# Performance work log

Hardware: AMD Instinct MI355X
Metric: run time of the kernel (lower is better)

## Reference

```python
import jax, jax.numpy as jnp
import numpy as np

N_NODES = 50000
BN_EPS = 1e-5


def setup_inputs() -> dict:
    key = jax.random.key(0)
    ks = jax.random.split(key, 10)
    n, e, d, L = N_NODES, 500000, 128, 2
    x = jax.random.normal(ks[0], (n, d), dtype=jnp.float32)
    edge_index = jax.random.randint(ks[1], (2, e), 0, n, dtype=jnp.int64)
    edge_attr = jax.random.normal(ks[2], (e, d), dtype=jnp.float32)
    W1 = jax.random.normal(ks[3], (L, d, d), dtype=jnp.float32) * 0.05
    b1 = jax.random.normal(ks[4], (L, d), dtype=jnp.float32) * 0.02
    gamma = 1.0 + 0.1 * jax.random.normal(ks[5], (L, d), dtype=jnp.float32)
    beta = 0.1 * jax.random.normal(ks[6], (L, d), dtype=jnp.float32)
    W2 = jax.random.normal(ks[7], (L, d, d), dtype=jnp.float32) * 0.05
    b2 = jax.random.normal(ks[8], (L, d), dtype=jnp.float32) * 0.02
    return {"x": x, "edge_index": edge_index, "edge_attr": edge_attr,
            "W1": W1, "b1": b1, "gamma": gamma, "beta": beta, "W2": W2, "b2": b2}


def _gine_layer(x, src, dst, edge_attr, W1l, b1l, gl, bl, W2l, b2l):
    # GINEConv message: relu(x_j + edge_attr), sum-aggregated to target nodes
    msg = jax.nn.relu(x[src] + edge_attr)              # [E, d]
    agg = jax.ops.segment_sum(msg, dst, num_segments=N_NODES)  # [N, d]
    h = (x + agg) @ W1l + b1l                           # eps=0 -> (1+eps)*x = x
    # BatchNorm1d over nodes (train-mode batch stats, biased var)
    mu = jnp.mean(h, axis=0)
    var = jnp.mean(jnp.square(h - mu), axis=0)
    h = (h - mu) * jax.lax.rsqrt(var + BN_EPS) * gl + bl
    h = jax.nn.relu(h)
    h = jax.nn.relu(h @ W2l + b2l)
    return jax.nn.relu(h)  # encoder's outer activation


def reference(x, edge_index, edge_attr, W1, b1, gamma, beta, W2, b2):
    src, dst = edge_index[0], edge_index[1]
    L = W1.shape[0]
    for l in range(L):
        x = _gine_layer(x, src, dst, edge_attr, W1[l], b1[l], gamma[l], beta[l], W2[l], b2[l])
    return x
```

## Files before the change

### kernel.cpp

```cpp
#include <hip/hip_runtime.h>

#define BN_EPS 1e-5f

using f4 = __attribute__((ext_vector_type(4))) float;
using h4 = __attribute__((ext_vector_type(4))) _Float16;

__device__ inline f4 relu4(f4 v) {
    v.x = fmaxf(v.x, 0.f); v.y = fmaxf(v.y, 0.f);
    v.z = fmaxf(v.z, 0.f); v.w = fmaxf(v.w, 0.f);
    return v;
}

__global__ __launch_bounds__(256) void detect_i64_kernel(const int* __restrict__ ei,
                                                         int* __restrict__ flag, int npairs,
                                                         int* __restrict__ deg, int N) {
    __shared__ int ok;
    if (threadIdx.x == 0) ok = 1;
    __syncthreads();
    bool bad = false;
    for (int i = threadIdx.x; i < npairs; i += 256)
        bad |= (ei[2 * i + 1] != 0);
    if (bad) ok = 0;
    int nq = N >> 2;
    int4* d4 = (int4*)deg;
    for (int i = threadIdx.x; i < nq; i += 256) d4[i] = make_int4(0, 0, 0, 0);
    for (int i = (nq << 2) + threadIdx.x; i < N; i += 256) deg[i] = 0;
    __syncthreads();
    if (threadIdx.x == 0) *flag = ok;
}

__global__ __launch_bounds__(256) void canon_kernel(const int* __restrict__ ei,
                                                    const int* __restrict__ flag,
                                                    int* __restrict__ canon,
                                                    int* __restrict__ deg, int n2, int E) {
    int i = blockIdx.x * 256 + threadIdx.x;
    if (i >= n2) return;
    int wide = *flag;
    int v = wide ? ei[2 * i] : ei[i];
    canon[i] = v;
    if (i >= E) atomicAdd(&deg[v], 1);
}

__global__ __launch_bounds__(256) void scan_blk_kernel(const int* __restrict__ deg,
                                                       int* __restrict__ rowptr,
                                                       int* __restrict__ partials, int N) {
    __shared__ int s[256];
    int b = blockIdx.x, t = threadIdx.x;
    int base = b * 1024 + t * 4;
    int4 v = make_int4(0, 0, 0, 0);
    if (base + 3 < N) v = *(const int4*)(deg + base);
    else {
        if (base < N) v.x = deg[base];
        if (base + 1 < N) v.y = deg[base + 1];
        if (base + 2 < N) v.z = deg[base + 2];
        if (base + 3 < N) v.w = deg[base + 3];
    }
    s[t] = v.x + v.y + v.z + v.w;
    __syncthreads();
    for (int off = 1; off < 256; off <<= 1) {
        int u = (t >= off) ? s[t - off] : 0;
        __syncthreads();
        s[t] += u;
        __syncthreads();
    }
    int excl = (t == 0) ? 0 : s[t - 1];
    int4 w;
    w.x = excl;
    w.y = excl + v.x;
    w.z = w.y + v.y;
    w.w = w.z + v.z;
    if (base + 3 < N) *(int4*)(rowptr + base) = w;
    else {
        if (base < N) rowptr[base] = w.x;
        if (base + 1 < N) rowptr[base + 1] = w.y;
        if (base + 2 < N) rowptr[base + 2] = w.z;
        if (base + 3 < N) rowptr[base + 3] = w.w;
    }
    if (t == 255) partials[b] = s[255];
}

__global__ __launch_bounds__(256) void scan_part_kernel(int* __restrict__ partials, int nb) {
    __shared__ int s[256];
    int t = threadIdx.x;
    if (nb <= 256) {
        s[t] = (t < nb) ? partials[t] : 0;
        __syncthreads();
        for (int off = 1; off < 256; off <<= 1) {
            int u = (t >= off) ? s[t - off] : 0;
            __syncthreads();
            s[t] += u;
            __syncthreads();
        }
        if (t < nb) partials[t] = (t == 0) ? 0 : s[t - 1];
    } else if (t == 0) {
        int run = 0;
        for (int i = 0; i < nb; ++i) { int d = partials[i]; partials[i] = run; run += d; }
    }
}

__global__ __launch_bounds__(256) void scan_add_kernel(int* __restrict__ rowptr,
                                                       int* __restrict__ cursor,
                                                       const int* __restrict__ partials,
                                                       float* __restrict__ sums, int nsum,
                                                       int N, int E) {
    int i = blockIdx.x * 256 + threadIdx.x;
    if (i < nsum) sums[i] = 0.f;
    if (i < N) {
        int v = rowptr[i] + partials[i >> 10];
        rowptr[i] = v;
        cursor[i] = v;
    }
    if (i == N) rowptr[N] = E;
}

__global__ __launch_bounds__(256) void fill_kernel(const int* __restrict__ src,
                                                   const int* __restrict__ dst,
                                                   int* __restrict__ cursor,
                                                   int2* __restrict__ pbuf, int E) {
    int e = blockIdx.x * 256 + threadIdx.x;
    if (e >= E) return;
    int d = dst[e];
    int pos = atomicAdd(&cursor[d], 1);
    pbuf[pos] = make_int2(e, src[e]);
}

template <int EAH>
__global__ __launch_bounds__(256) void gg1_kernel(const float* __restrict__ x,
                                                  const float* __restrict__ ea,
                                                  _Float16* __restrict__ eah,
                                                  const int* __restrict__ rowptr,
                                                  const int2* __restrict__ pbuf,
                                                  const float* __restrict__ W,
                                                  const float* __restrict__ bias,
                                                  float* __restrict__ sums,
                                                  float* __restrict__ out, int N) {
    __shared__ float sA[64][132];
    __shared__ float sW[32][128];
    int t = threadIdx.x;
    int rbase = blockIdx.x * 64;
    int f = t & 31, g = t >> 5;

    for (int it = 0; it < 8; ++it) {
        int r = g * 8 + it;
        int n = rbase + r;
        f4 acc0 = {0.f, 0.f, 0.f, 0.f};
        f4 acc1 = {0.f, 0.f, 0.f, 0.f};
        f4 acc2 = {0.f, 0.f, 0.f, 0.f};
        f4 acc3 = {0.f, 0.f, 0.f, 0.f};
        if (n < N) {
            acc0 = ((const f4*)(x + (size_t)n * 128))[f];
            int lo = rowptr[n], hi = rowptr[n + 1];
            int i = lo;
            if (EAH == 1) {
                const h4* ep = (const h4*)eah;
                for (; i + 4 <= hi; i += 4) {
                    int2 q0 = pbuf[i];
                    int2 q1 = pbuf[i + 1];
                    int2 q2 = pbuf[i + 2];
                    int2 q3 = pbuf[i + 3];
                    f4 xa = ((const f4*)(x + (size_t)q0.y * 128))[f];
                    h4 ha = __builtin_nontemporal_load(ep + (size_t)i * 32 + f);
                    f4 xb = ((const f4*)(x + (size_t)q1.y * 128))[f];
                    h4 hb = __builtin_nontemporal_load(ep + (size_t)(i + 1) * 32 + f);
                    f4 xc = ((const f4*)(x + (size_t)q2.y * 128))[f];
                    h4 hc = __builtin_nontemporal_load(ep + (size_t)(i + 2) * 32 + f);
                    f4 xd = ((const f4*)(x + (size_t)q3.y * 128))[f];
                    h4 hd = __builtin_nontemporal_load(ep + (size_t)(i + 3) * 32 + f);
                    acc0 += relu4(xa + __builtin_convertvector(ha, f4));
                    acc1 += relu4(xb + __builtin_convertvector(hb, f4));
                    acc2 += relu4(xc + __builtin_convertvector(hc, f4));
                    acc3 += relu4(xd + __builtin_convertvector(hd, f4));
                }
                for (; i < hi; ++i) {
                    int2 q0 = pbuf[i];
                    f4 xa = ((const f4*)(x + (size_t)q0.y * 128))[f];
                    h4 ha = __builtin_nontemporal_load(ep + (size_t)i * 32 + f);
                    acc0 += relu4(xa + __builtin_convertvector(ha, f4));
                }
            } else {
                for (; i + 4 <= hi; i += 4) {
                    int2 q0 = pbuf[i];
                    int2 q1 = pbuf[i + 1];
                    int2 q2 = pbuf[i + 2];
                    int2 q3 = pbuf[i + 3];
                    f4 xa = ((const f4*)(x + (size_t)q0.y * 128))[f];
                    f4 aa = __builtin_nontemporal_load(((const f4*)(ea + (size_t)q0.x * 128)) + f);
                    f4 xb = ((const f4*)(x + (size_t)q1.y * 128))[f];
                    f4 ab = __builtin_nontemporal_load(((const f4*)(ea + (size_t)q1.x * 128)) + f);
                    f4 xc = ((const f4*)(x + (size_t)q2.y * 128))[f];
                    f4 ac = __builtin_nontemporal_load(((const f4*)(ea + (size_t)q2.x * 128)) + f);
                    f4 xd = ((const f4*)(x + (size_t)q3.y * 128))[f];
                    f4 ad = __builtin_nontemporal_load(((const f4*)(ea + (size_t)q3.x * 128)) + f);
                    if (EAH == 0) {
                        h4* ep = (h4*)eah;
                        __builtin_nontemporal_store(__builtin_convertvector(aa, h4), ep + (size_t)i * 32 + f);
                        __builtin_nontemporal_store(__builtin_convertvector(ab, h4), ep + (size_t)(i + 1) * 32 + f);
                        __builtin_nontemporal_store(__builtin_convertvector(ac, h4), ep + (size_t)(i + 2) * 32 + f);
                        __builtin_nontemporal_store(__builtin_convertvector(ad, h4), ep + (size_t)(i + 3) * 32 + f);
                    }
                    acc0 += relu4(xa + aa);
                    acc1 += relu4(xb + ab);
                    acc2 += relu4(xc + ac);
                    acc3 += relu4(xd + ad);
                }
                for (; i < hi; ++i) {
                    int2 q0 = pbuf[i];
                    f4 xa = ((const f4*)(x + (size_t)q0.y * 128))[f];
                    f4 aa = __builtin_nontemporal_load(((const f4*)(ea + (size_t)q0.x * 128)) + f);
                    if (EAH == 0) {
                        h4* ep = (h4*)eah;
                        __builtin_nontemporal_store(__builtin_convertvector(aa, h4), ep + (size_t)i * 32 + f);
                    }
                    acc0 += relu4(xa + aa);
                }
            }
        }
        f4 rv = (acc0 + acc1) + (acc2 + acc3);
        *(f4*)&sA[r][f * 4] = rv;
    }

    float acc[4][8];
#pragma unroll
    for (int r = 0; r < 4; ++r)
#pragma unroll
        for (int c = 0; c < 8; ++c) acc[r][c] = 0.f;

    int cg = t & 15, rg = t >> 4;
    int c0a = cg * 4;
    int c0b = 64 + cg * 4;

    for (int kc = 0; kc < 4; ++kc) {
        __syncthreads();
#pragma unroll
        for (int pass = 0; pass < 4; ++pass) {
            int kk = (t >> 5) + pass * 8;
            int k = kc * 32 + kk;
            float4 w = reinterpret_cast<const float4*>(W + (size_t)k * 128)[t & 31];
            *reinterpret_cast<float4*>(&sW[kk][(t & 31) * 4]) = w;
        }
        __syncthreads();
#pragma unroll
        for (int kk0 = 0; kk0 < 32; kk0 += 4) {
            float4 a[4];
#pragma unroll
            for (int r = 0; r < 4; ++r)
                a[r] = *reinterpret_cast<const float4*>(&sA[rg * 4 + r][kc * 32 + kk0]);
#pragma unroll
            for (int j = 0; j < 4; ++j) {
                float4 w0 = *reinterpret_cast<const float4*>(&sW[kk0 + j][c0a]);
                float4 w1 = *reinterpret_cast<const float4*>(&sW[kk0 + j][c0b]);
#pragma unroll
                for (int r = 0; r < 4; ++r) {
                    float av = (j == 0) ? a[r].x : (j == 1) ? a[r].y : (j == 2) ? a[r].z : a[r].w;
                    acc[r][0] += av * w0.x;
                    acc[r][1] += av * w0.y;
                    acc[r][2] += av * w0.z;
                    acc[r][3] += av * w0.w;
                    acc[r][4] += av * w1.x;
                    acc[r][5] += av * w1.y;
                    acc[r][6] += av * w1.z;
                    acc[r][7] += av * w1.w;
                }
            }
        }
    }

    float4 b0 = *reinterpret_cast<const float4*>(bias + c0a);
    float4 b1v = *reinterpret_cast<const float4*>(bias + c0b);
    float cs[8], cs2[8];
#pragma unroll
    for (int j = 0; j < 8; ++j) { cs[j] = 0.f; cs2[j] = 0.f; }

#pragma unroll
    for (int r = 0; r < 4; ++r) {
        int row = rbase + rg * 4 + r;
        if (row >= N) continue;
        float4 o0, o1;
        o0.x = acc[r][0] + b0.x;  o0.y = acc[r][1] + b0.y;
        o0.z = acc[r][2] + b0.z;  o0.w = acc[r][3] + b0.w;
        o1.x = acc[r][4] + b1v.x; o1.y = acc[r][5] + b1v.y;
        o1.z = acc[r][6] + b1v.z; o1.w = acc[r][7] + b1v.w;
        cs[0] += o0.x; cs2[0] += o0.x * o0.x;
        cs[1] += o0.y; cs2[1] += o0.y * o0.y;
        cs[2] += o0.z; cs2[2] += o0.z * o0.z;
        cs[3] += o0.w; cs2[3] += o0.w * o0.w;
        cs[4] += o1.x; cs2[4] += o1.x * o1.x;
        cs[5] += o1.y; cs2[5] += o1.y * o1.y;
        cs[6] += o1.z; cs2[6] += o1.z * o1.z;
        cs[7] += o1.w; cs2[7] += o1.w * o1.w;
        *reinterpret_cast<float4*>(out + (size_t)row * 128 + c0a) = o0;
        *reinterpret_cast<float4*>(out + (size_t)row * 128 + c0b) = o1;
    }

    __syncthreads();
    float* red = &sA[0][0];
    float* red2 = red + 2048;
    int base = (rg * 16 + cg) * 8;
#pragma unroll
    for (int j = 0; j < 8; ++j) { red[base + j] = cs[j]; red2[base + j] = cs2[j]; }
    __syncthreads();
    if (t < 128) {
        int cgj = (t & 63) >> 2;
        int j = (t & 3) + ((t >> 6) << 2);
        float s = 0.f, s2 = 0.f;
#pragma unroll
        for (int rr = 0; rr < 16; ++rr) {
            s += red[(rr * 16 + cgj) * 8 + j];
            s2 += red2[(rr * 16 + cgj) * 8 + j];
        }
        unsafeAtomicAdd(&sums[t], s);
        unsafeAtomicAdd(&sums[128 + t], s2);
    }
}

__global__ __launch_bounds__(256) void gemm2_kernel(const float* __restrict__ A,
                                                    const float* __restrict__ W,
                                                    const float* __restrict__ bias,
                                                    const float* __restrict__ sums,
                                                    const float* __restrict__ gamma,
                                                    const float* __restrict__ beta,
                                                    float* __restrict__ out, int N,
                                                    float invN) {
    __shared__ float sA[64][132];
    __shared__ float sW[32][128];
    __shared__ float sScale[128];
    __shared__ float sShift[128];
    int t = threadIdx.x;
    int rbase = blockIdx.x * 64;

    if (t < 128) {
        float mean = sums[t] * invN;
        float var = sums[128 + t] * invN - mean * mean;
        float inv = rsqrtf(var + BN_EPS);
        float sc = gamma[t] * inv;
        sScale[t] = sc;
        sShift[t] = beta[t] - mean * sc;
    }
    __syncthreads();

    {
        int colq = t & 31;
        int r0 = t >> 5;
        float4 s4 = reinterpret_cast<const float4*>(sScale)[colq];
        float4 sh4 = reinterpret_cast<const float4*>(sShift)[colq];
#pragma unroll
        for (int it = 0; it < 8; ++it) {
            int r = r0 + it * 8;
            int row = rbase + r;
            float4 v = make_float4(0.f, 0.f, 0.f, 0.f);
            if (row < N) {
                float4 a = reinterpret_cast<const float4*>(A + (size_t)row * 128)[colq];
                v.x = fmaxf(a.x * s4.x + sh4.x, 0.f);
                v.y = fmaxf(a.y * s4.y + sh4.y, 0.f);
                v.z = fmaxf(a.z * s4.z + sh4.z, 0.f);
                v.w = fmaxf(a.w * s4.w + sh4.w, 0.f);
            }
            *reinterpret_cast<float4*>(&sA[r][colq * 4]) = v;
        }
    }

    float acc[4][8];
#pragma unroll
    for (int r = 0; r < 4; ++r)
#pragma unroll
        for (int c = 0; c < 8; ++c) acc[r][c] = 0.f;

    int cg = t & 15, rg = t >> 4;
    int c0a = cg * 4;
    int c0b = 64 + cg * 4;

    for (int kc = 0; kc < 4; ++kc) {
        __syncthreads();
#pragma unroll
        for (int pass = 0; pass < 4; ++pass) {
            int kk = (t >> 5) + pass * 8;
            int k = kc * 32 + kk;
            float4 w = reinterpret_cast<const float4*>(W + (size_t)k * 128)[t & 31];
            *reinterpret_cast<float4*>(&sW[kk][(t & 31) * 4]) = w;
        }
        __syncthreads();
#pragma unroll
        for (int kk0 = 0; kk0 < 32; kk0 += 4) {
            float4 a[4];
#pragma unroll
            for (int r = 0; r < 4; ++r)
                a[r] = *reinterpret_cast<const float4*>(&sA[rg * 4 + r][kc * 32 + kk0]);
#pragma unroll
            for (int j = 0; j < 4; ++j) {
                float4 w0 = *reinterpret_cast<const float4*>(&sW[kk0 + j][c0a]);
                float4 w1 = *reinterpret_cast<const float4*>(&sW[kk0 + j][c0b]);
#pragma unroll
                for (int r = 0; r < 4; ++r) {
                    float av = (j == 0) ? a[r].x : (j == 1) ? a[r].y : (j == 2) ? a[r].z : a[r].w;
                    acc[r][0] += av * w0.x;
                    acc[r][1] += av * w0.y;
                    acc[r][2] += av * w0.z;
                    acc[r][3] += av * w0.w;
                    acc[r][4] += av * w1.x;
                    acc[r][5] += av * w1.y;
                    acc[r][6] += av * w1.z;
                    acc[r][7] += av * w1.w;
                }
            }
        }
    }

    float4 b0 = *reinterpret_cast<const float4*>(bias + c0a);
    float4 b1v = *reinterpret_cast<const float4*>(bias + c0b);
#pragma unroll
    for (int r = 0; r < 4; ++r) {
        int row = rbase + rg * 4 + r;
        if (row >= N) continue;
        float4 o0, o1;
        o0.x = fmaxf(acc[r][0] + b0.x, 0.f);  o0.y = fmaxf(acc[r][1] + b0.y, 0.f);
        o0.z = fmaxf(acc[r][2] + b0.z, 0.f);  o0.w = fmaxf(acc[r][3] + b0.w, 0.f);
        o1.x = fmaxf(acc[r][4] + b1v.x, 0.f); o1.y = fmaxf(acc[r][5] + b1v.y, 0.f);
        o1.z = fmaxf(acc[r][6] + b1v.z, 0.f); o1.w = fmaxf(acc[r][7] + b1v.w, 0.f);
        *reinterpret_cast<float4*>(out + (size_t)row * 128 + c0a) = o0;
        *reinterpret_cast<float4*>(out + (size_t)row * 128 + c0b) = o1;
    }
}

extern "C" void kernel_launch(void* const* d_in, const int* in_sizes, int n_in,
                              void* d_out, int out_size, void* d_ws, size_t ws_size,
                              hipStream_t stream) {
    const float* x     = (const float*)d_in[0];
    const int*   ei    = (const int*)d_in[1];
    const float* ea    = (const float*)d_in[2];
    const float* W1    = (const float*)d_in[3];
    const float* b1    = (const float*)d_in[4];
    const float* gamma = (const float*)d_in[5];
    const float* beta  = (const float*)d_in[6];
    const float* W2    = (const float*)d_in[7];
    const float* b2    = (const float*)d_in[8];

    int N = in_sizes[0] / 128;
    int E = in_sizes[2] / 128;
    int L = in_sizes[3] / (128 * 128);

    size_t NF = (size_t)N * 128;
    float*     h      = (float*)d_ws;
    float*     sums   = h + NF;
    _Float16*  eah    = (_Float16*)(sums + 256 * L);
    int*       canon  = (int*)(eah + (size_t)E * 128);
    int*       deg    = canon + (size_t)2 * E;
    int*       rowptr = deg + N;
    int*       cursor = rowptr + N + 2;
    int2*      pbuf   = (int2*)(cursor + N);
    int*       partials = (int*)(pbuf + E);
    int*       flag   = partials + ((N + 1023) / 1024) + 1;

    int npairs = (E < 4096) ? E : 4096;
    detect_i64_kernel<<<1, 256, 0, stream>>>(ei, flag, npairs, deg, N);
    int E2 = 2 * E;
    canon_kernel<<<(E2 + 255) / 256, 256, 0, stream>>>(ei, flag, canon, deg, E2, E);
    const int* src = canon;
    const int* dst = canon + E;

    int nb = (N + 1023) / 1024;
    scan_blk_kernel<<<nb, 256, 0, stream>>>(deg, rowptr, partials, N);
    scan_part_kernel<<<1, 256, 0, stream>>>(partials, nb);
    scan_add_kernel<<<(N + 256) / 256, 256, 0, stream>>>(rowptr, cursor, partials,
                                                         sums, 256 * L, N, E);
    int eBlocks = (E + 255) / 256;
    fill_kernel<<<eBlocks, 256, 0, stream>>>(src, dst, cursor, pbuf, E);

    int gemmBlocks = (N + 63) / 64;
    float invN = 1.0f / (float)N;
    const float* xin = x;
    for (int l = 0; l < L; ++l) {
        float* xout = (float*)d_out;
        const float* W1l = W1 + (size_t)l * 16384;
        const float* b1l = b1 + (size_t)l * 128;
        float* sums_l = sums + (size_t)l * 256;
        if (l == 0) {
            if (L > 1)
                gg1_kernel<0><<<gemmBlocks, 256, 0, stream>>>(xin, ea, eah, rowptr, pbuf,
                                                              W1l, b1l, sums_l, h, N);
            else
                gg1_kernel<2><<<gemmBlocks, 256, 0, stream>>>(xin, ea, eah, rowptr, pbuf,
                                                              W1l, b1l, sums_l, h, N);
        } else {
            gg1_kernel<1><<<gemmBlocks, 256, 0, stream>>>(xin, ea, eah, rowptr, pbuf,
                                                          W1l, b1l, sums_l, h, N);
        }
        gemm2_kernel<<<gemmBlocks, 256, 0, stream>>>(h, W2 + (size_t)l * 16384,
                                                     b2 + (size_t)l * 128, sums_l,
                                                     gamma + (size_t)l * 128,
                                                     beta + (size_t)l * 128, xout, N, invN);
        xin = xout;
    }
}
```

Measured before the change: 708.1 us.

## Split fused gather-GEMM into gather, permute, and standalone GEMM kernels

```diff
diff --git a/kernel.cpp b/kernel.cpp
--- a/kernel.cpp
+++ b/kernel.cpp
@@ -116,107 +116,93 @@
 __global__ __launch_bounds__(256) void fill_kernel(const int* __restrict__ src,
                                                    const int* __restrict__ dst,
                                                    int* __restrict__ cursor,
-                                                   int2* __restrict__ pbuf, int E) {
+                                                   int* __restrict__ sbuf,
+                                                   int* __restrict__ epos, int E) {
     int e = blockIdx.x * 256 + threadIdx.x;
     if (e >= E) return;
     int d = dst[e];
     int pos = atomicAdd(&cursor[d], 1);
-    pbuf[pos] = make_int2(e, src[e]);
-}
-
-template <int EAH>
-__global__ __launch_bounds__(256) void gg1_kernel(const float* __restrict__ x,
-                                                  const float* __restrict__ ea,
-                                                  _Float16* __restrict__ eah,
-                                                  const int* __restrict__ rowptr,
-                                                  const int2* __restrict__ pbuf,
-                                                  const float* __restrict__ W,
-                                                  const float* __restrict__ bias,
-                                                  float* __restrict__ sums,
-                                                  float* __restrict__ out, int N) {
+    sbuf[pos] = src[e];
+    epos[e] = pos;
+}
+
+__global__ __launch_bounds__(256) void permute_kernel(const float* __restrict__ ea,
+                                                      const int* __restrict__ epos,
+                                                      _Float16* __restrict__ eah, int E) {
+    int t = blockIdx.x * 256 + threadIdx.x;
+    int e = t >> 5;
+    if (e >= E) return;
+    int f = t & 31;
+    int pos = epos[e];
+    f4 v = __builtin_nontemporal_load(((const f4*)(ea + (size_t)e * 128)) + f);
+    ((h4*)eah)[(size_t)pos * 32 + f] = __builtin_convertvector(v, h4);
+}
+
+__global__ __launch_bounds__(256) void gather_kernel(const float* __restrict__ x,
+                                                     const _Float16* __restrict__ eah,
+                                                     const int* __restrict__ rowptr,
+                                                     const int* __restrict__ sbuf,
+                                                     float* __restrict__ aggx, int N) {
+    int t = blockIdx.x * 256 + threadIdx.x;
+    int n = t >> 5;
+    if (n >= N) return;
+    int f = t & 31;
+    int lo = rowptr[n], hi = rowptr[n + 1];
+    const h4* ep = (const h4*)eah;
+    f4 acc0 = ((const f4*)(x + (size_t)n * 128))[f];
+    f4 acc1 = {0.f, 0.f, 0.f, 0.f};
+    f4 acc2 = {0.f, 0.f, 0.f, 0.f};
+    f4 acc3 = {0.f, 0.f, 0.f, 0.f};
+    int i = lo;
+    for (; i + 4 <= hi; i += 4) {
+        int s0 = sbuf[i];
+        int s1 = sbuf[i + 1];
+        int s2 = sbuf[i + 2];
+        int s3 = sbuf[i + 3];
+        f4 xa = ((const f4*)(x + (size_t)s0 * 128))[f];
+        h4 ha = ep[(size_t)i * 32 + f];
+        f4 xb = ((const f4*)(x + (size_t)s1 * 128))[f];
+        h4 hb = ep[(size_t)(i + 1) * 32 + f];
+        f4 xc = ((const f4*)(x + (size_t)s2 * 128))[f];
+        h4 hc = ep[(size_t)(i + 2) * 32 + f];
+        f4 xd = ((const f4*)(x + (size_t)s3 * 128))[f];
+        h4 hd = ep[(size_t)(i + 3) * 32 + f];
+        acc0 += relu4(xa + __builtin_convertvector(ha, f4));
+        acc1 += relu4(xb + __builtin_convertvector(hb, f4));
+        acc2 += relu4(xc + __builtin_convertvector(hc, f4));
+        acc3 += relu4(xd + __builtin_convertvector(hd, f4));
+    }
+    for (; i < hi; ++i) {
+        int s0 = sbuf[i];
+        f4 xa = ((const f4*)(x + (size_t)s0 * 128))[f];
+        h4 ha = ep[(size_t)i * 32 + f];
+        acc0 += relu4(xa + __builtin_convertvector(ha, f4));
+    }
+    f4 r = (acc0 + acc1) + (acc2 + acc3);
+    ((f4*)(aggx + (size_t)n * 128))[f] = r;
+}
+
+__global__ __launch_bounds__(256) void gemm1_kernel(const float* A,
+                                                    const float* __restrict__ W,
+                                                    const float* __restrict__ bias,
+                                                    float* __restrict__ sums,
+                                                    float* out, int N) {
     __shared__ float sA[64][132];
     __shared__ float sW[32][128];
     int t = threadIdx.x;
     int rbase = blockIdx.x * 64;
-    int f = t & 31, g = t >> 5;
-
-    for (int it = 0; it < 8; ++it) {
-        int r = g * 8 + it;
-        int n = rbase + r;
-        f4 acc0 = {0.f, 0.f, 0.f, 0.f};
-        f4 acc1 = {0.f, 0.f, 0.f, 0.f};
-        f4 acc2 = {0.f, 0.f, 0.f, 0.f};
-        f4 acc3 = {0.f, 0.f, 0.f, 0.f};
-        if (n < N) {
-            acc0 = ((const f4*)(x + (size_t)n * 128))[f];
-            int lo = rowptr[n], hi = rowptr[n + 1];
-            int i = lo;
-            if (EAH == 1) {
-                const h4* ep = (const h4*)eah;
-                for (; i + 4 <= hi; i += 4) {
-                    int2 q0 = pbuf[i];
-                    int2 q1 = pbuf[i + 1];
-                    int2 q2 = pbuf[i + 2];
-                    int2 q3 = pbuf[i + 3];
-                    f4 xa = ((const f4*)(x + (size_t)q0.y * 128))[f];
-                    h4 ha = __builtin_nontemporal_load(ep + (size_t)i * 32 + f);
-                    f4 xb = ((const f4*)(x + (size_t)q1.y * 128))[f];
-                    h4 hb = __builtin_nontemporal_load(ep + (size_t)(i + 1) * 32 + f);
-                    f4 xc = ((const f4*)(x + (size_t)q2.y * 128))[f];
-                    h4 hc = __builtin_nontemporal_load(ep + (size_t)(i + 2) * 32 + f);
-                    f4 xd = ((const f4*)(x + (size_t)q3.y * 128))[f];
-                    h4 hd = __builtin_nontemporal_load(ep + (size_t)(i + 3) * 32 + f);
-                    acc0 += relu4(xa + __builtin_convertvector(ha, f4));
-                    acc1 += relu4(xb + __builtin_convertvector(hb, f4));
-                    acc2 += relu4(xc + __builtin_convertvector(hc, f4));
-                    acc3 += relu4(xd + __builtin_convertvector(hd, f4));
-                }
-                for (; i < hi; ++i) {
-                    int2 q0 = pbuf[i];
-                    f4 xa = ((const f4*)(x + (size_t)q0.y * 128))[f];
-                    h4 ha = __builtin_nontemporal_load(ep + (size_t)i * 32 + f);
-                    acc0 += relu4(xa + __builtin_convertvector(ha, f4));
-                }
-            } else {
-                for (; i + 4 <= hi; i += 4) {
-                    int2 q0 = pbuf[i];
-                    int2 q1 = pbuf[i + 1];
-                    int2 q2 = pbuf[i + 2];
-                    int2 q3 = pbuf[i + 3];
-                    f4 xa = ((const f4*)(x + (size_t)q0.y * 128))[f];
-                    f4 aa = __builtin_nontemporal_load(((const f4*)(ea + (size_t)q0.x * 128)) + f);
-                    f4 xb = ((const f4*)(x + (size_t)q1.y * 128))[f];
-                    f4 ab = __builtin_nontemporal_load(((const f4*)(ea + (size_t)q1.x * 128)) + f);
-                    f4 xc = ((const f4*)(x + (size_t)q2.y * 128))[f];
-                    f4 ac = __builtin_nontemporal_load(((const f4*)(ea + (size_t)q2.x * 128)) + f);
-                    f4 xd = ((const f4*)(x + (size_t)q3.y * 128))[f];
-                    f4 ad = __builtin_nontemporal_load(((const f4*)(ea + (size_t)q3.x * 128)) + f);
-                    if (EAH == 0) {
-                        h4* ep = (h4*)eah;
-                        __builtin_nontemporal_store(__builtin_convertvector(aa, h4), ep + (size_t)i * 32 + f);
-                        __builtin_nontemporal_store(__builtin_convertvector(ab, h4), ep + (size_t)(i + 1) * 32 + f);
-                        __builtin_nontemporal_store(__builtin_convertvector(ac, h4), ep + (size_t)(i + 2) * 32 + f);
-                        __builtin_nontemporal_store(__builtin_convertvector(ad, h4), ep + (size_t)(i + 3) * 32 + f);
-                    }
-                    acc0 += relu4(xa + aa);
-                    acc1 += relu4(xb + ab);
-                    acc2 += relu4(xc + ac);
-                    acc3 += relu4(xd + ad);
-                }
-                for (; i < hi; ++i) {
-                    int2 q0 = pbuf[i];
-                    f4 xa = ((const f4*)(x + (size_t)q0.y * 128))[f];
-                    f4 aa = __builtin_nontemporal_load(((const f4*)(ea + (size_t)q0.x * 128)) + f);
-                    if (EAH == 0) {
-                        h4* ep = (h4*)eah;
-                        __builtin_nontemporal_store(__builtin_convertvector(aa, h4), ep + (size_t)i * 32 + f);
-                    }
-                    acc0 += relu4(xa + aa);
-                }
-            }
-        }
-        f4 rv = (acc0 + acc1) + (acc2 + acc3);
-        *(f4*)&sA[r][f * 4] = rv;
+
+    {
+        int colq = t & 31;
+        int r0 = t >> 5;
+#pragma unroll
+        for (int it = 0; it < 8; ++it) {
+            int r = r0 + it * 8;
+            int row = rbase + r;
+            float4 v = make_float4(0.f, 0.f, 0.f, 0.f);
+            if (row < N) v = reinterpret_cast<const float4*>(A + (size_t)row * 128)[colq];
+            *reinterpret_cast<float4*>(&sA[r][colq * 4]) = v;
+        }
     }
 
     float acc[4][8];
@@ -439,15 +425,16 @@
     int L = in_sizes[3] / (128 * 128);
 
     size_t NF = (size_t)N * 128;
-    float*     h      = (float*)d_ws;
-    float*     sums   = h + NF;
+    float*     buf    = (float*)d_ws;
+    float*     sums   = buf + NF;
     _Float16*  eah    = (_Float16*)(sums + 256 * L);
     int*       canon  = (int*)(eah + (size_t)E * 128);
     int*       deg    = canon + (size_t)2 * E;
     int*       rowptr = deg + N;
     int*       cursor = rowptr + N + 2;
-    int2*      pbuf   = (int2*)(cursor + N);
-    int*       partials = (int*)(pbuf + E);
+    int*       sbuf   = cursor + N;
+    int*       epos   = sbuf + E;
+    int*       partials = epos + E;
     int*       flag   = partials + ((N + 1023) / 1024) + 1;
 
     int npairs = (E < 4096) ? E : 4096;
@@ -463,28 +450,21 @@
     scan_add_kernel<<<(N + 256) / 256, 256, 0, stream>>>(rowptr, cursor, partials,
                                                          sums, 256 * L, N, E);
     int eBlocks = (E + 255) / 256;
-    fill_kernel<<<eBlocks, 256, 0, stream>>>(src, dst, cursor, pbuf, E);
-
+    fill_kernel<<<eBlocks, 256, 0, stream>>>(src, dst, cursor, sbuf, epos, E);
+    int pBlocks = (int)(((size_t)E * 32 + 255) / 256);
+    permute_kernel<<<pBlocks, 256, 0, stream>>>(ea, epos, eah, E);
+
+    int gatherBlocks = (N * 32 + 255) / 256;
     int gemmBlocks = (N + 63) / 64;
     float invN = 1.0f / (float)N;
     const float* xin = x;
     for (int l = 0; l < L; ++l) {
         float* xout = (float*)d_out;
-        const float* W1l = W1 + (size_t)l * 16384;
-        const float* b1l = b1 + (size_t)l * 128;
         float* sums_l = sums + (size_t)l * 256;
-        if (l == 0) {
-            if (L > 1)
-                gg1_kernel<0><<<gemmBlocks, 256, 0, stream>>>(xin, ea, eah, rowptr, pbuf,
-                                                              W1l, b1l, sums_l, h, N);
-            else
-                gg1_kernel<2><<<gemmBlocks, 256, 0, stream>>>(xin, ea, eah, rowptr, pbuf,
-                                                              W1l, b1l, sums_l, h, N);
-        } else {
-            gg1_kernel<1><<<gemmBlocks, 256, 0, stream>>>(xin, ea, eah, rowptr, pbuf,
-                                                          W1l, b1l, sums_l, h, N);
-        }
-        gemm2_kernel<<<gemmBlocks, 256, 0, stream>>>(h, W2 + (size_t)l * 16384,
+        gather_kernel<<<gatherBlocks, 256, 0, stream>>>(xin, eah, rowptr, sbuf, buf, N);
+        gemm1_kernel<<<gemmBlocks, 256, 0, stream>>>(buf, W1 + (size_t)l * 16384,
+                                                     b1 + (size_t)l * 128, sums_l, buf, N);
+        gemm2_kernel<<<gemmBlocks, 256, 0, stream>>>(buf, W2 + (size_t)l * 16384,
                                                      b2 + (size_t)l * 128, sums_l,
                                                      gamma + (size_t)l * 128,
                                                      beta + (size_t)l * 128, xout, N, invN);
```

New measurement: 694.5 us. Within noise of the previous version (-1.9%).

## Split fused gather+GEMM1 into a wide gather kernel and a separate GEMM1

Applied to the files above, without the earlier changes.

```diff
diff --git a/kernel.cpp b/kernel.cpp
--- a/kernel.cpp
+++ b/kernel.cpp
@@ -124,99 +124,108 @@
     pbuf[pos] = make_int2(e, src[e]);
 }
 
-template <int EAH>
-__global__ __launch_bounds__(256) void gg1_kernel(const float* __restrict__ x,
-                                                  const float* __restrict__ ea,
-                                                  _Float16* __restrict__ eah,
-                                                  const int* __restrict__ rowptr,
-                                                  const int2* __restrict__ pbuf,
-                                                  const float* __restrict__ W,
-                                                  const float* __restrict__ bias,
-                                                  float* __restrict__ sums,
-                                                  float* __restrict__ out, int N) {
+template <int MODE>
+__global__ __launch_bounds__(256) void gather_kernel(const float* __restrict__ x,
+                                                     const float* __restrict__ ea,
+                                                     _Float16* __restrict__ eah,
+                                                     const int* __restrict__ rowptr,
+                                                     const int2* __restrict__ pbuf,
+                                                     float* __restrict__ aggx, int N) {
+    int t = blockIdx.x * 256 + threadIdx.x;
+    int n = t >> 5;
+    if (n >= N) return;
+    int f = t & 31;
+    int lo = rowptr[n], hi = rowptr[n + 1];
+    f4 acc0 = ((const f4*)(x + (size_t)n * 128))[f];
+    f4 acc1 = {0.f, 0.f, 0.f, 0.f};
+    f4 acc2 = {0.f, 0.f, 0.f, 0.f};
+    f4 acc3 = {0.f, 0.f, 0.f, 0.f};
+    int i = lo;
+    if (MODE == 1) {
+        const h4* ep = (const h4*)eah;
+        for (; i + 4 <= hi; i += 4) {
+            int2 q0 = pbuf[i];
+            int2 q1 = pbuf[i + 1];
+            int2 q2 = pbuf[i + 2];
+            int2 q3 = pbuf[i + 3];
+            f4 xa = ((const f4*)(x + (size_t)q0.y * 128))[f];
+            h4 ha = ep[(size_t)i * 32 + f];
+            f4 xb = ((const f4*)(x + (size_t)q1.y * 128))[f];
+            h4 hb = ep[(size_t)(i + 1) * 32 + f];
+            f4 xc = ((const f4*)(x + (size_t)q2.y * 128))[f];
+            h4 hc = ep[(size_t)(i + 2) * 32 + f];
+            f4 xd = ((const f4*)(x + (size_t)q3.y * 128))[f];
+            h4 hd = ep[(size_t)(i + 3) * 32 + f];
+            acc0 += relu4(xa + __builtin_convertvector(ha, f4));
+            acc1 += relu4(xb + __builtin_convertvector(hb, f4));
+            acc2 += relu4(xc + __builtin_convertvector(hc, f4));
+            acc3 += relu4(xd + __builtin_convertvector(hd, f4));
+        }
+        for (; i < hi; ++i) {
+            int2 q0 = pbuf[i];
+            f4 xa = ((const f4*)(x + (size_t)q0.y * 128))[f];
+            h4 ha = ep[(size_t)i * 32 + f];
+            acc0 += relu4(xa + __builtin_convertvector(ha, f4));
+        }
+    } else {
+        h4* ep = (h4*)eah;
+        for (; i + 4 <= hi; i += 4) {
+            int2 q0 = pbuf[i];
+            int2 q1 = pbuf[i + 1];
+            int2 q2 = pbuf[i + 2];
+            int2 q3 = pbuf[i + 3];
+            f4 xa = ((const f4*)(x + (size_t)q0.y * 128))[f];
+            f4 aa = __builtin_nontemporal_load(((const f4*)(ea + (size_t)q0.x * 128)) + f);
+            f4 xb = ((const f4*)(x + (size_t)q1.y * 128))[f];
+            f4 ab = __builtin_nontemporal_load(((const f4*)(ea + (size_t)q1.x * 128)) + f);
+            f4 xc = ((const f4*)(x + (size_t)q2.y * 128))[f];
+            f4 ac = __builtin_nontemporal_load(((const f4*)(ea + (size_t)q2.x * 128)) + f);
+            f4 xd = ((const f4*)(x + (size_t)q3.y * 128))[f];
+            f4 ad = __builtin_nontemporal_load(((const f4*)(ea + (size_t)q3.x * 128)) + f);
+            if (MODE == 0) {
+                ep[(size_t)i * 32 + f] = __builtin_convertvector(aa, h4);
+                ep[(size_t)(i + 1) * 32 + f] = __builtin_convertvector(ab, h4);
+                ep[(size_t)(i + 2) * 32 + f] = __builtin_convertvector(ac, h4);
+                ep[(size_t)(i + 3) * 32 + f] = __builtin_convertvector(ad, h4);
+            }
+            acc0 += relu4(xa + aa);
+            acc1 += relu4(xb + ab);
+            acc2 += relu4(xc + ac);
+            acc3 += relu4(xd + ad);
+        }
+        for (; i < hi; ++i) {
+            int2 q0 = pbuf[i];
+            f4 xa = ((const f4*)(x + (size_t)q0.y * 128))[f];
+            f4 aa = __builtin_nontemporal_load(((const f4*)(ea + (size_t)q0.x * 128)) + f);
+            if (MODE == 0) ep[(size_t)i * 32 + f] = __builtin_convertvector(aa, h4);
+            acc0 += relu4(xa + aa);
+        }
+    }
+    f4 r = (acc0 + acc1) + (acc2 + acc3);
+    ((f4*)(aggx + (size_t)n * 128))[f] = r;
+}
+
+__global__ __launch_bounds__(256) void gemm1_kernel(const float* A,
+                                                    const float* __restrict__ W,
+                                                    const float* __restrict__ bias,
+                                                    float* __restrict__ sums,
+                                                    float* out, int N) {
     __shared__ float sA[64][132];
     __shared__ float sW[32][128];
     int t = threadIdx.x;
     int rbase = blockIdx.x * 64;
-    int f = t & 31, g = t >> 5;
-
-    for (int it = 0; it < 8; ++it) {
-        int r = g * 8 + it;
-        int n = rbase + r;
-        f4 acc0 = {0.f, 0.f, 0.f, 0.f};
-        f4 acc1 = {0.f, 0.f, 0.f, 0.f};
-        f4 acc2 = {0.f, 0.f, 0.f, 0.f};
-        f4 acc3 = {0.f, 0.f, 0.f, 0.f};
-        if (n < N) {
-            acc0 = ((const f4*)(x + (size_t)n * 128))[f];
-            int lo = rowptr[n], hi = rowptr[n + 1];
-            int i = lo;
-            if (EAH == 1) {
-                const h4* ep = (const h4*)eah;
-                for (; i + 4 <= hi; i += 4) {
-                    int2 q0 = pbuf[i];
-                    int2 q1 = pbuf[i + 1];
-                    int2 q2 = pbuf[i + 2];
-                    int2 q3 = pbuf[i + 3];
-                    f4 xa = ((const f4*)(x + (size_t)q0.y * 128))[f];
-                    h4 ha = __builtin_nontemporal_load(ep + (size_t)i * 32 + f);
-                    f4 xb = ((const f4*)(x + (size_t)q1.y * 128))[f];
-                    h4 hb = __builtin_nontemporal_load(ep + (size_t)(i + 1) * 32 + f);
-                    f4 xc = ((const f4*)(x + (size_t)q2.y * 128))[f];
-                    h4 hc = __builtin_nontemporal_load(ep + (size_t)(i + 2) * 32 + f);
-                    f4 xd = ((const f4*)(x + (size_t)q3.y * 128))[f];
-                    h4 hd = __builtin_nontemporal_load(ep + (size_t)(i + 3) * 32 + f);
-                    acc0 += relu4(xa + __builtin_convertvector(ha, f4));
-                    acc1 += relu4(xb + __builtin_convertvector(hb, f4));
-                    acc2 += relu4(xc + __builtin_convertvector(hc, f4));
-                    acc3 += relu4(xd + __builtin_convertvector(hd, f4));
-                }
-                for (; i < hi; ++i) {
-                    int2 q0 = pbuf[i];
-                    f4 xa = ((const f4*)(x + (size_t)q0.y * 128))[f];
-                    h4 ha = __builtin_nontemporal_load(ep + (size_t)i * 32 + f);
-                    acc0 += relu4(xa + __builtin_convertvector(ha, f4));
-                }
-            } else {
-                for (; i + 4 <= hi; i += 4) {
-                    int2 q0 = pbuf[i];
-                    int2 q1 = pbuf[i + 1];
-                    int2 q2 = pbuf[i + 2];
-                    int2 q3 = pbuf[i + 3];
-                    f4 xa = ((const f4*)(x + (size_t)q0.y * 128))[f];
-                    f4 aa = __builtin_nontemporal_load(((const f4*)(ea + (size_t)q0.x * 128)) + f);
-                    f4 xb = ((const f4*)(x + (size_t)q1.y * 128))[f];
-                    f4 ab = __builtin_nontemporal_load(((const f4*)(ea + (size_t)q1.x * 128)) + f);
-                    f4 xc = ((const f4*)(x + (size_t)q2.y * 128))[f];
-                    f4 ac = __builtin_nontemporal_load(((const f4*)(ea + (size_t)q2.x * 128)) + f);
-                    f4 xd = ((const f4*)(x + (size_t)q3.y * 128))[f];
-                    f4 ad = __builtin_nontemporal_load(((const f4*)(ea + (size_t)q3.x * 128)) + f);
-                    if (EAH == 0) {
-                        h4* ep = (h4*)eah;
-                        __builtin_nontemporal_store(__builtin_convertvector(aa, h4), ep + (size_t)i * 32 + f);
-                        __builtin_nontemporal_store(__builtin_convertvector(ab, h4), ep + (size_t)(i + 1) * 32 + f);
-                        __builtin_nontemporal_store(__builtin_convertvector(ac, h4), ep + (size_t)(i + 2) * 32 + f);
-                        __builtin_nontemporal_store(__builtin_convertvector(ad, h4), ep + (size_t)(i + 3) * 32 + f);
-                    }
-                    acc0 += relu4(xa + aa);
-                    acc1 += relu4(xb + ab);
-                    acc2 += relu4(xc + ac);
-                    acc3 += relu4(xd + ad);
-                }
-                for (; i < hi; ++i) {
-                    int2 q0 = pbuf[i];
-                    f4 xa = ((const f4*)(x + (size_t)q0.y * 128))[f];
-                    f4 aa = __builtin_nontemporal_load(((const f4*)(ea + (size_t)q0.x * 128)) + f);
-                    if (EAH == 0) {
-                        h4* ep = (h4*)eah;
-                        __builtin_nontemporal_store(__builtin_convertvector(aa, h4), ep + (size_t)i * 32 + f);
-                    }
-                    acc0 += relu4(xa + aa);
-                }
-            }
-        }
-        f4 rv = (acc0 + acc1) + (acc2 + acc3);
-        *(f4*)&sA[r][f * 4] = rv;
+
+    {
+        int colq = t & 31;
+        int r0 = t >> 5;
+#pragma unroll
+        for (int it = 0; it < 8; ++it) {
+            int r = r0 + it * 8;
+            int row = rbase + r;
+            float4 v = make_float4(0.f, 0.f, 0.f, 0.f);
+            if (row < N) v = reinterpret_cast<const float4*>(A + (size_t)row * 128)[colq];
+            *reinterpret_cast<float4*>(&sA[r][colq * 4]) = v;
+        }
     }
 
     float acc[4][8];
@@ -439,8 +448,8 @@
     int L = in_sizes[3] / (128 * 128);
 
     size_t NF = (size_t)N * 128;
-    float*     h      = (float*)d_ws;
-    float*     sums   = h + NF;
+    float*     buf    = (float*)d_ws;
+    float*     sums   = buf + NF;
     _Float16*  eah    = (_Float16*)(sums + 256 * L);
     int*       canon  = (int*)(eah + (size_t)E * 128);
     int*       deg    = canon + (size_t)2 * E;
@@ -465,26 +474,27 @@
     int eBlocks = (E + 255) / 256;
     fill_kernel<<<eBlocks, 256, 0, stream>>>(src, dst, cursor, pbuf, E);
 
+    int gatherBlocks = (N * 32 + 255) / 256;
     int gemmBlocks = (N + 63) / 64;
     float invN = 1.0f / (float)N;
     const float* xin = x;
     for (int l = 0; l < L; ++l) {
         float* xout = (float*)d_out;
-        const float* W1l = W1 + (size_t)l * 16384;
-        const float* b1l = b1 + (size_t)l * 128;
         float* sums_l = sums + (size_t)l * 256;
         if (l == 0) {
             if (L > 1)
-                gg1_kernel<0><<<gemmBlocks, 256, 0, stream>>>(xin, ea, eah, rowptr, pbuf,
-                                                              W1l, b1l, sums_l, h, N);
+                gather_kernel<0><<<gatherBlocks, 256, 0, stream>>>(xin, ea, eah, rowptr,
+                                                                   pbuf, buf, N);
             else
-                gg1_kernel<2><<<gemmBlocks, 256, 0, stream>>>(xin, ea, eah, rowptr, pbuf,
-                                                              W1l, b1l, sums_l, h, N);
+                gather_kernel<2><<<gatherBlocks, 256, 0, stream>>>(xin, ea, eah, rowptr,
+                                                                   pbuf, buf, N);
         } else {
-            gg1_kernel<1><<<gemmBlocks, 256, 0, stream>>>(xin, ea, eah, rowptr, pbuf,
-                                                          W1l, b1l, sums_l, h, N);
-        }
-        gemm2_kernel<<<gemmBlocks, 256, 0, stream>>>(h, W2 + (size_t)l * 16384,
+            gather_kernel<1><<<gatherBlocks, 256, 0, stream>>>(xin, ea, eah, rowptr,
+                                                               pbuf, buf, N);
+        }
+        gemm1_kernel<<<gemmBlocks, 256, 0, stream>>>(buf, W1 + (size_t)l * 16384,
+                                                     b1 + (size_t)l * 128, sums_l, buf, N);
+        gemm2_kernel<<<gemmBlocks, 256, 0, stream>>>(buf, W2 + (size_t)l * 16384,
                                                      b2 + (size_t)l * 128, sums_l,
                                                      gamma + (size_t)l * 128,
                                                      beta + (size_t)l * 128, xout, N, invN);
```

New measurement: 673.3 us. 1.05x faster.
